# Performance work log

Measured on AMD Instinct MI355X. Metric: run time of the kernel, lower is better.

## Reference

```python
import jax, jax.numpy as jnp
import numpy as np

N_NODES = 50000
N_RAND_EDGES = 800000
N_GRAPHS = 64
IN_DIM, HID, HEADS = 1024, 64, 4
NEG_SLOPE = 0.2  # PyG GATConv default


def setup_inputs() -> dict:
    key = jax.random.key(0)
    ks = jax.random.split(key, 16)
    x = jax.random.normal(ks[0], (N_NODES, IN_DIM), dtype=jnp.float32)
    src = jax.random.randint(ks[1], (N_RAND_EDGES,), 0, N_NODES, dtype=jnp.int32)
    dst = jax.random.randint(ks[2], (N_RAND_EDGES,), 0, N_NODES, dtype=jnp.int32)
    loop = jnp.arange(N_NODES, dtype=jnp.int32)
    # PyG GATConv adds self-loops by default; bake them into edge_index.
    edge_index = jnp.stack([jnp.concatenate([src, loop]), jnp.concatenate([dst, loop])])
    batch = jnp.sort(jax.random.randint(ks[3], (N_NODES,), 0, N_GRAPHS, dtype=jnp.int32))
    s = 0.05
    W1 = jax.random.normal(ks[4], (IN_DIM, HEADS * HID), dtype=jnp.float32) * s
    att_src1 = jax.random.normal(ks[5], (HEADS, HID), dtype=jnp.float32) * s
    att_dst1 = jax.random.normal(ks[6], (HEADS, HID), dtype=jnp.float32) * s
    b1 = jnp.zeros((HEADS * HID,), dtype=jnp.float32)
    W2 = jax.random.normal(ks[7], (HEADS * HID, HID), dtype=jnp.float32) * s
    att_src2 = jax.random.normal(ks[8], (1, HID), dtype=jnp.float32) * s
    att_dst2 = jax.random.normal(ks[9], (1, HID), dtype=jnp.float32) * s
    b2 = jnp.zeros((HID,), dtype=jnp.float32)
    fc_w = jax.random.normal(ks[10], (HID, 2), dtype=jnp.float32) * s
    fc_b = jnp.zeros((2,), dtype=jnp.float32)
    return {"x": x, "edge_index": edge_index, "batch": batch,
            "W1": W1, "att_src1": att_src1, "att_dst1": att_dst1, "b1": b1,
            "W2": W2, "att_src2": att_src2, "att_dst2": att_dst2, "b2": b2,
            "fc_w": fc_w, "fc_b": fc_b}


def gat_conv(x, src, dst, W, a_src, a_dst, b):
    """PyG GATConv (eval mode, concat=True). x:[N,Fin] -> [N, H*C]."""
    N = x.shape[0]
    H, C = a_src.shape
    h = (x @ W).reshape(N, H, C)                      # [N,H,C]
    al_s = jnp.einsum('nhc,hc->nh', h, a_src)         # [N,H]
    al_d = jnp.einsum('nhc,hc->nh', h, a_dst)
    e = jax.nn.leaky_relu(al_s[src] + al_d[dst], NEG_SLOPE)   # [E,H]
    # segment-softmax over edges grouped by destination node
    m = jax.ops.segment_max(e, dst, num_segments=N)           # [N,H]
    w = jnp.exp(e - m[dst])
    denom = jax.ops.segment_sum(w, dst, num_segments=N)
    alpha = w / denom[dst]                                    # [E,H]
    msg = h[src] * alpha[:, :, None]                          # [E,H,C]
    out = jax.ops.segment_sum(msg, dst, num_segments=N)       # [N,H,C]
    return out.reshape(N, H * C) + b


def reference(x, edge_index, batch, W1, att_src1, att_dst1, b1,
              W2, att_src2, att_dst2, b2, fc_w, fc_b):
    src, dst = edge_index[0], edge_index[1]
    # dropout is identity in eval mode
    h = jax.nn.elu(gat_conv(x, src, dst, W1, att_src1, att_dst1, b1))
    h = jax.nn.elu(gat_conv(h, src, dst, W2, att_src2, att_dst2, b2))
    # global mean pool over graphs
    sums = jax.ops.segment_sum(h, batch, num_segments=N_GRAPHS)          # [G,HID]
    cnt = jax.ops.segment_sum(jnp.ones((h.shape[0],), h.dtype), batch,
                              num_segments=N_GRAPHS)
    pooled = sums / jnp.maximum(cnt, 1.0)[:, None]
    return pooled @ fc_w + fc_b                                          # [G,2]
```

## Files before the change

kernel.cpp:

```cpp
#include <hip/hip_runtime.h>
#include <hip/hip_bf16.h>

#define NNODES   50000
#define NGRAPHS  64
#define INDIM    1024
#define HIDC     64
#define HEADS1   4
#define F1       (HEADS1*HIDC)
#define NEG_SLOPE 0.2f

#define WS_COUNTS   0
#define WS_ZEROLEN  50000
#define WS_INDPTR   54208
#define WS_CURSOR   104256
#define WS_CSRSRC   154304
#define WS_CSRDST   1004304
#define WS_BSUM     1854304
#define WS_ALS1     1854368
#define WS_ALD1     2054368
#define WS_ALS2     2254368
#define WS_ALD2     2304368
#define WS_BP       2354368
#define WS_BP2      2485440
#define WS_H1B      2493632
#define WS_X2B      8893632
#define WS_H2B      15293632
#define WS_HFIN     16893632

typedef __attribute__((ext_vector_type(8))) short bf16x8;
typedef __attribute__((ext_vector_type(4))) float f32x4;

__device__ __forceinline__ ushort f2bf(float f) {
    union { float f; uint u; } v; v.f = f;
    uint r = v.u + 0x7fff + ((v.u >> 16) & 1);
    return (ushort)(r >> 16);
}
__device__ __forceinline__ float bf2f(ushort u) {
    union { uint u; float f; } v; v.u = (uint)u << 16; return v.f;
}

__global__ void prep_kernel(const float* __restrict__ W1, const float* __restrict__ W2,
                            ushort* __restrict__ Bp1, ushort* __restrict__ Bp2,
                            int* __restrict__ counts) {
    int b = blockIdx.x;
    int tid = threadIdx.x;
    if (b < 1024) {
        int o = b * 256 + tid;
        int j = o & 7;
        int lane = (o >> 3) & 63;
        int kchunk = (o >> 9) & 31;
        int ntile = o >> 14;
        int k = kchunk * 32 + (lane >> 4) * 8 + j;
        int n = ntile * 16 + (lane & 15);
        Bp1[o] = f2bf(W1[k * 256 + n]);
    } else if (b < 1088) {
        int o = (b - 1024) * 256 + tid;
        int j = o & 7;
        int lane = (o >> 3) & 63;
        int kchunk = (o >> 9) & 7;
        int ntile = o >> 12;
        int k = kchunk * 32 + (lane >> 4) * 8 + j;
        int n = ntile * 16 + (lane & 15);
        Bp2[o] = f2bf(W2[k * 64 + n]);
    } else {
        int i = (b - 1088) * 256 + tid;
        if (i < NNODES) counts[i] = 0;
    }
}

__global__ void hist_kernel(const int* __restrict__ dst, int* __restrict__ counts, int E) {
    int i = blockIdx.x * blockDim.x + threadIdx.x;
    if (i < E) atomicAdd(&counts[dst[i]], 1);
}

__global__ __launch_bounds__(1024) void scan1_kernel(const int* __restrict__ counts,
                                                     int* __restrict__ indptr,
                                                     int* __restrict__ bsum, int N) {
    __shared__ int sm[1024];
    int b = blockIdx.x;
    int i = b * 1024 + (int)threadIdx.x;
    int v = (i < N) ? counts[i] : 0;
    sm[threadIdx.x] = v;
    __syncthreads();
    for (int off = 1; off < 1024; off <<= 1) {
        int t = (threadIdx.x >= (unsigned)off) ? sm[threadIdx.x - off] : 0;
        __syncthreads();
        sm[threadIdx.x] += t;
        __syncthreads();
    }
    if (i < N) indptr[i + 1] = sm[threadIdx.x];
    if (threadIdx.x == 1023) bsum[b] = sm[1023];
}

__global__ void scan2_kernel(int* __restrict__ bsum, int nb) {
    int lane = threadIdx.x;
    int v = (lane < nb) ? bsum[lane] : 0;
    int orig = v;
    #pragma unroll
    for (int off = 1; off < 64; off <<= 1) {
        int t = __shfl_up(v, off, 64);
        if (lane >= off) v += t;
    }
    if (lane < nb) bsum[lane] = v - orig;
}

__global__ __launch_bounds__(1024) void scan3_kernel(const int* __restrict__ counts,
                                                     int* __restrict__ indptr,
                                                     int* __restrict__ cursor,
                                                     const int* __restrict__ bsum, int N) {
    int i = blockIdx.x * 1024 + (int)threadIdx.x;
    if (i == 0) indptr[0] = 0;
    if (i < N) {
        int incl = indptr[i + 1] + bsum[blockIdx.x];
        indptr[i + 1] = incl;
        cursor[i] = incl - counts[i];
    }
}

__global__ void fill_kernel(const int* __restrict__ src, const int* __restrict__ dst,
                            int* __restrict__ cursor, int* __restrict__ csr_src, int E) {
    int i = blockIdx.x * blockDim.x + threadIdx.x;
    if (i < E) {
        int d = dst[i];
        int pos = atomicAdd(&cursor[d], 1);
        csr_src[pos] = src[i];
    }
}

__global__ __launch_bounds__(256) void gemm1_mfma(const float* __restrict__ A,
                                                  const ushort* __restrict__ Bp,
                                                  ushort* __restrict__ C,
                                                  const float* __restrict__ asrc,
                                                  const float* __restrict__ adst,
                                                  float* __restrict__ als,
                                                  float* __restrict__ ald,
                                                  int M) {
    __shared__ __align__(16) ushort Atile[2][128 * 32];
    const int K = 1024, N = 256;
    int tid = threadIdx.x;
    int lane = tid & 63;
    int w = tid >> 6;
    int wm = w >> 1, wn = w & 1;
    int m0 = blockIdx.x * 128;

    const float* srow[4];
    int soff[4];
    #pragma unroll
    for (int l = 0; l < 4; ++l) {
        int slot = l * 256 + tid;
        int m = slot >> 3, hc = slot & 7;
        int c = hc >> 1;
        int row = m0 + m; if (row >= M) row = M - 1;
        srow[l] = A + (size_t)row * K + hc * 4;
        soff[l] = (m * 4 + (c ^ ((m >> 1) & 3))) * 8 + (hc & 1) * 4;
    }
    int afrag_off[4];
    #pragma unroll
    for (int mt = 0; mt < 4; ++mt) {
        int r = wm * 64 + mt * 16 + (lane & 15);
        int cq = lane >> 4;
        afrag_off[mt] = (r * 4 + (cq ^ ((r >> 1) & 3))) * 8;
    }
    const ushort* bbase[8];
    #pragma unroll
    for (int nt = 0; nt < 8; ++nt) {
        int ntile = wn * 8 + nt;
        bbase[nt] = Bp + ((size_t)(ntile * 32) * 64 + lane) * 8;
    }

    f32x4 acc[4][8] = {};
    float4 v[4];
    #pragma unroll
    for (int l = 0; l < 4; ++l) v[l] = *(const float4*)(srow[l]);

    for (int kc = 0; kc < 32; ++kc) {
        ushort* At = Atile[kc & 1];
        #pragma unroll
        for (int l = 0; l < 4; ++l) {
            ushort4 b;
            b.x = f2bf(v[l].x); b.y = f2bf(v[l].y);
            b.z = f2bf(v[l].z); b.w = f2bf(v[l].w);
            *(ushort4*)&At[soff[l]] = b;
        }
        __syncthreads();
        if (kc < 31) {
            #pragma unroll
            for (int l = 0; l < 4; ++l)
                v[l] = *(const float4*)(srow[l] + (kc + 1) * 32);
        }
        bf16x8 afr[4];
        #pragma unroll
        for (int mt = 0; mt < 4; ++mt)
            afr[mt] = *(const bf16x8*)&At[afrag_off[mt]];
        #pragma unroll
        for (int nt = 0; nt < 8; ++nt) {
            bf16x8 bfr = *(const bf16x8*)(bbase[nt] + (size_t)kc * 64 * 8);
            #pragma unroll
            for (int mt = 0; mt < 4; ++mt)
                acc[mt][nt] = __builtin_amdgcn_mfma_f32_16x16x32_bf16(afr[mt], bfr, acc[mt][nt], 0, 0, 0);
        }
    }

    float a_s[8], a_d[8];
    #pragma unroll
    for (int nt = 0; nt < 8; ++nt) {
        int col = wn * 128 + nt * 16 + (lane & 15);
        a_s[nt] = asrc[col];
        a_d[nt] = adst[col];
    }
    #pragma unroll
    for (int mt = 0; mt < 4; ++mt) {
        #pragma unroll
        for (int nt = 0; nt < 8; ++nt) {
            int col = wn * 128 + nt * 16 + (lane & 15);
            #pragma unroll
            for (int r = 0; r < 4; ++r) {
                int row = m0 + wm * 64 + mt * 16 + (lane >> 4) * 4 + r;
                if (row < M) C[(size_t)row * N + col] = f2bf(acc[mt][nt][r]);
            }
        }
        #pragma unroll
        for (int hg = 0; hg < 2; ++hg) {
            int head = wn * 2 + hg;
            #pragma unroll
            for (int r = 0; r < 4; ++r) {
                int row = m0 + wm * 64 + mt * 16 + (lane >> 4) * 4 + r;
                float s = 0.f, d = 0.f;
                #pragma unroll
                for (int q = 0; q < 4; ++q) {
                    float c = acc[mt][4 * hg + q][r];
                    s = fmaf(c, a_s[4 * hg + q], s);
                    d = fmaf(c, a_d[4 * hg + q], d);
                }
                #pragma unroll
                for (int off = 1; off < 16; off <<= 1) {
                    s += __shfl_xor(s, off, 64);
                    d += __shfl_xor(d, off, 64);
                }
                if ((lane & 15) == 0 && row < M) {
                    als[row * 4 + head] = s;
                    ald[row * 4 + head] = d;
                }
            }
        }
    }
}

__global__ __launch_bounds__(256) void gemm2_mfma(const ushort* __restrict__ Ab,
                                                  const ushort* __restrict__ Bp,
                                                  ushort* __restrict__ C,
                                                  const float* __restrict__ asrc,
                                                  const float* __restrict__ adst,
                                                  float* __restrict__ als,
                                                  float* __restrict__ ald,
                                                  int M) {
    int tid = threadIdx.x;
    int lane = tid & 63;
    int w = tid >> 6;
    int m0 = blockIdx.x * 128 + w * 32;

    f32x4 acc[2][4] = {};
    #pragma unroll 2
    for (int kc = 0; kc < 8; ++kc) {
        bf16x8 afr[2];
        #pragma unroll
        for (int mt = 0; mt < 2; ++mt) {
            int r = m0 + mt * 16 + (lane & 15);
            if (r >= M) r = M - 1;
            afr[mt] = *(const bf16x8*)&Ab[(size_t)r * 256 + kc * 32 + (lane >> 4) * 8];
        }
        #pragma unroll
        for (int nt = 0; nt < 4; ++nt) {
            bf16x8 bfr = *(const bf16x8*)&Bp[((nt * 8 + kc) * 64 + lane) * 8];
            acc[0][nt] = __builtin_amdgcn_mfma_f32_16x16x32_bf16(afr[0], bfr, acc[0][nt], 0, 0, 0);
            acc[1][nt] = __builtin_amdgcn_mfma_f32_16x16x32_bf16(afr[1], bfr, acc[1][nt], 0, 0, 0);
        }
    }
    float a_s[4], a_d[4];
    #pragma unroll
    for (int nt = 0; nt < 4; ++nt) {
        a_s[nt] = asrc[nt * 16 + (lane & 15)];
        a_d[nt] = adst[nt * 16 + (lane & 15)];
    }
    #pragma unroll
    for (int mt = 0; mt < 2; ++mt) {
        #pragma unroll
        for (int nt = 0; nt < 4; ++nt) {
            int col = nt * 16 + (lane & 15);
            #pragma unroll
            for (int r = 0; r < 4; ++r) {
                int row = m0 + mt * 16 + (lane >> 4) * 4 + r;
                if (row < M) C[(size_t)row * 64 + col] = f2bf(acc[mt][nt][r]);
            }
        }
        #pragma unroll
        for (int r = 0; r < 4; ++r) {
            int row = m0 + mt * 16 + (lane >> 4) * 4 + r;
            float s = 0.f, d = 0.f;
            #pragma unroll
            for (int nt = 0; nt < 4; ++nt) {
                float c = acc[mt][nt][r];
                s = fmaf(c, a_s[nt], s);
                d = fmaf(c, a_d[nt], d);
            }
            #pragma unroll
            for (int off = 1; off < 16; off <<= 1) {
                s += __shfl_xor(s, off, 64);
                d += __shfl_xor(d, off, 64);
            }
            if ((lane & 15) == 0 && row < M) {
                als[row] = s;
                ald[row] = d;
            }
        }
    }
}

__device__ __forceinline__ float wave_reduce_sum(float v) {
    #pragma unroll
    for (int off = 32; off > 0; off >>= 1) v += __shfl_xor(v, off, 64);
    return v;
}

__device__ __forceinline__ float edge_w(float e) {
    e = (e > 0.f) ? e : NEG_SLOPE * e;
    return __expf(e);
}

__global__ __launch_bounds__(256) void agg1_kernel(const ushort* __restrict__ h,
                                                   const float* __restrict__ als,
                                                   const float* __restrict__ ald,
                                                   const int* __restrict__ indptr,
                                                   const int* __restrict__ csr_src,
                                                   const float* __restrict__ bias,
                                                   ushort* __restrict__ out, int N) {
    __shared__ int   s_s[4][64];
    __shared__ float s_w[4][64][4];
    int wv   = threadIdx.x >> 6;
    int lane = threadIdx.x & 63;
    int n = blockIdx.x * 4 + wv;
    if (n >= N) return;
    int hd = lane >> 4;
    int beg = indptr[n], end = indptr[n + 1];
    float4 aldv = *(const float4*)&ald[n * 4];

    float4 acc = make_float4(0.f, 0.f, 0.f, 0.f);
    float den = 0.f;

    for (int base = beg; base < end; base += 64) {
        int cnt = end - base; if (cnt > 64) cnt = 64;
        if (lane < cnt) {
            int s = csr_src[base + lane];
            s_s[wv][lane] = s;
            float4 av = *(const float4*)&als[s * 4];
            s_w[wv][lane][0] = edge_w(av.x + aldv.x);
            s_w[wv][lane][1] = edge_w(av.y + aldv.y);
            s_w[wv][lane][2] = edge_w(av.z + aldv.z);
            s_w[wv][lane][3] = edge_w(av.w + aldv.w);
        }
        #pragma unroll 4
        for (int e = 0; e < cnt; ++e) {
            int s = s_s[wv][e];
            float wt = s_w[wv][e][hd];
            ushort4 a = *(const ushort4*)&h[(size_t)s * 256 + lane * 4];
            acc.x = fmaf(wt, bf2f(a.x), acc.x);
            acc.y = fmaf(wt, bf2f(a.y), acc.y);
            acc.z = fmaf(wt, bf2f(a.z), acc.z);
            acc.w = fmaf(wt, bf2f(a.w), acc.w);
            den += wt;
        }
    }

    float inv = 1.0f / den;
    float4 bv = *(const float4*)&bias[lane * 4];
    float o0 = acc.x * inv + bv.x, o1 = acc.y * inv + bv.y;
    float o2 = acc.z * inv + bv.z, o3 = acc.w * inv + bv.w;
    o0 = (o0 > 0.f) ? o0 : (__expf(o0) - 1.0f);
    o1 = (o1 > 0.f) ? o1 : (__expf(o1) - 1.0f);
    o2 = (o2 > 0.f) ? o2 : (__expf(o2) - 1.0f);
    o3 = (o3 > 0.f) ? o3 : (__expf(o3) - 1.0f);
    ushort4 ob; ob.x = f2bf(o0); ob.y = f2bf(o1); ob.z = f2bf(o2); ob.w = f2bf(o3);
    *(ushort4*)&out[(size_t)n * 256 + lane * 4] = ob;
}

__global__ __launch_bounds__(256) void agg2_kernel(const ushort* __restrict__ h,
                                                   const float* __restrict__ als,
                                                   const float* __restrict__ ald,
                                                   const int* __restrict__ indptr,
                                                   const int* __restrict__ csr_src,
                                                   const float* __restrict__ bias,
                                                   float* __restrict__ out, int N) {
    __shared__ int   s_s[8][32];
    __shared__ float s_w[8][32];
    int tid = threadIdx.x;
    int sl  = tid >> 5;
    int l32 = tid & 31;
    int n = blockIdx.x * 8 + sl;
    if (n >= N) return;
    int beg = indptr[n], end = indptr[n + 1];
    float ald_n = ald[n];

    float2 acc = make_float2(0.f, 0.f);
    float den = 0.f;

    for (int base = beg; base < end; base += 32) {
        int cnt = end - base; if (cnt > 32) cnt = 32;
        if (l32 < cnt) {
            int s = csr_src[base + l32];
            s_s[sl][l32] = s;
            s_w[sl][l32] = edge_w(als[s] + ald_n);
        }
        #pragma unroll 4
        for (int e = 0; e < cnt; ++e) {
            int s = s_s[sl][e];
            float wt = s_w[sl][e];
            ushort2 hv = *(const ushort2*)&h[(size_t)s * 64 + l32 * 2];
            acc.x = fmaf(wt, bf2f(hv.x), acc.x);
            acc.y = fmaf(wt, bf2f(hv.y), acc.y);
            den += wt;
        }
    }

    float inv = 1.0f / den;
    float o0 = acc.x * inv + bias[l32 * 2];
    float o1 = acc.y * inv + bias[l32 * 2 + 1];
    o0 = (o0 > 0.f) ? o0 : (__expf(o0) - 1.0f);
    o1 = (o1 > 0.f) ? o1 : (__expf(o1) - 1.0f);
    *(float2*)&out[(size_t)n * 64 + l32 * 2] = make_float2(o0, o1);
}

__global__ __launch_bounds__(256) void pool_fc_kernel(const float* __restrict__ hfin,
                                                      const int* __restrict__ batch,
                                                      const float* __restrict__ fc_w,
                                                      const float* __restrict__ fc_b,
                                                      float* __restrict__ out, int N) {
    __shared__ float lacc[4][64];
    int g = blockIdx.x;
    int beg, end;
    {
        int lo = 0, hi = N;
        while (lo < hi) { int mid = (lo + hi) >> 1; if (batch[mid] < g) lo = mid + 1; else hi = mid; }
        beg = lo;
        lo = beg; hi = N;
        while (lo < hi) { int mid = (lo + hi) >> 1; if (batch[mid] < g + 1) lo = mid + 1; else hi = mid; }
        end = lo;
    }
    int lane = threadIdx.x & 63;
    int wv = threadIdx.x >> 6;
    float acc = 0.f;
    for (int n = beg + wv; n < end; n += 4)
        acc += hfin[(size_t)n * 64 + lane];
    lacc[wv][lane] = acc;
    __syncthreads();
    if (wv == 0) {
        float s = lacc[0][lane] + lacc[1][lane] + lacc[2][lane] + lacc[3][lane];
        float cnt = fmaxf((float)(end - beg), 1.0f);
        float pooled = s / cnt;
        float p0 = wave_reduce_sum(pooled * fc_w[lane * 2 + 0]);
        float p1 = wave_reduce_sum(pooled * fc_w[lane * 2 + 1]);
        if (lane == 0) {
            out[g * 2 + 0] = p0 + fc_b[0];
            out[g * 2 + 1] = p1 + fc_b[1];
        }
    }
}

extern "C" void kernel_launch(void* const* d_in, const int* in_sizes, int n_in,
                              void* d_out, int out_size, void* d_ws, size_t ws_size,
                              hipStream_t stream) {
    const float* x      = (const float*)d_in[0];
    const int*   ei     = (const int*)d_in[1];
    const int*   batch  = (const int*)d_in[2];
    const float* W1     = (const float*)d_in[3];
    const float* asrc1  = (const float*)d_in[4];
    const float* adst1  = (const float*)d_in[5];
    const float* b1     = (const float*)d_in[6];
    const float* W2     = (const float*)d_in[7];
    const float* asrc2  = (const float*)d_in[8];
    const float* adst2  = (const float*)d_in[9];
    const float* b2     = (const float*)d_in[10];
    const float* fc_w   = (const float*)d_in[11];
    const float* fc_b   = (const float*)d_in[12];
    float* out          = (float*)d_out;

    const int N = in_sizes[2];
    const int E = in_sizes[1] / 2;
    const int* src = ei;
    const int* dst = ei + E;

    float* ws = (float*)d_ws;
    int*    counts  = (int*)(ws + WS_COUNTS);
    int*    indptr  = (int*)(ws + WS_INDPTR);
    int*    cursor  = (int*)(ws + WS_CURSOR);
    int*    csr_src = (int*)(ws + WS_CSRSRC);
    int*    bsum    = (int*)(ws + WS_BSUM);
    float*  al_s1   = ws + WS_ALS1;
    float*  al_d1   = ws + WS_ALD1;
    float*  al_s2   = ws + WS_ALS2;
    float*  al_d2   = ws + WS_ALD2;
    ushort* bp      = (ushort*)(ws + WS_BP);
    ushort* bp2     = (ushort*)(ws + WS_BP2);
    ushort* h1b     = (ushort*)(ws + WS_H1B);
    ushort* x2b     = (ushort*)(ws + WS_X2B);
    ushort* h2b     = (ushort*)(ws + WS_H2B);
    float*  hfin    = ws + WS_HFIN;

    const int nb = (N + 1023) / 1024;

    prep_kernel<<<1284, 256, 0, stream>>>(W1, W2, bp, bp2, counts);
    hist_kernel<<<(E + 255) / 256, 256, 0, stream>>>(dst, counts, E);
    scan1_kernel<<<nb, 1024, 0, stream>>>(counts, indptr, bsum, N);
    scan2_kernel<<<1, 64, 0, stream>>>(bsum, nb);
    scan3_kernel<<<nb, 1024, 0, stream>>>(counts, indptr, cursor, bsum, N);
    fill_kernel<<<(E + 255) / 256, 256, 0, stream>>>(src, dst, cursor, csr_src, E);
    gemm1_mfma<<<(N + 127) / 128, 256, 0, stream>>>(
        x, bp, h1b, asrc1, adst1, al_s1, al_d1, N);
    agg1_kernel<<<(N + 3) / 4, 256, 0, stream>>>(h1b, al_s1, al_d1, indptr, csr_src, b1, x2b, N);
    gemm2_mfma<<<(N + 127) / 128, 256, 0, stream>>>(
        x2b, bp2, h2b, asrc2, adst2, al_s2, al_d2, N);
    agg2_kernel<<<(N + 7) / 8, 256, 0, stream>>>(h2b, al_s2, al_d2, indptr, csr_src, b2, hfin, N);
    pool_fc_kernel<<<NGRAPHS, 256, 0, stream>>>(hfin, batch, fc_w, fc_b, out, N);
}
```

Baseline: 575.9 us.

## Pre-convert x to bf16 in separate pass and drop LDS staging in gemm1

Adds a standalone kernel converting the fp32 node features to bf16 in workspace, then gemm1 reads bf16 A fragments directly from global memory instead of converting and staging through double-buffered shared memory with barriers. This removes in-loop conversion and syncthreads from the GEMM. It adds an extra full pass over the large input (read fp32, write bf16, read bf16 again) and relies on cache for the uncoalesced per-lane row fragment loads.

```diff
diff --git a/kernel.cpp b/kernel.cpp
--- a/kernel.cpp
+++ b/kernel.cpp
@@ -26,6 +26,7 @@
 #define WS_X2B      8893632
 #define WS_H2B      15293632
 #define WS_HFIN     16893632
+#define WS_XB       20093632
 
 typedef __attribute__((ext_vector_type(8))) short bf16x8;
 typedef __attribute__((ext_vector_type(4))) float f32x4;
@@ -37,6 +38,20 @@
 }
 __device__ __forceinline__ float bf2f(ushort u) {
     union { uint u; float f; } v; v.u = (uint)u << 16; return v.f;
+}
+
+__global__ void cvt_x_kernel(const float* __restrict__ x, ushort* __restrict__ xb,
+                             long n8) {
+    long i = blockIdx.x * (long)blockDim.x + threadIdx.x;
+    long stride = (long)gridDim.x * blockDim.x;
+    for (; i < n8; i += stride) {
+        const float4* p = (const float4*)(x + i * 8);
+        float4 a = p[0], b = p[1];
+        union { ushort u[8]; uint4 v; } o;
+        o.u[0] = f2bf(a.x); o.u[1] = f2bf(a.y); o.u[2] = f2bf(a.z); o.u[3] = f2bf(a.w);
+        o.u[4] = f2bf(b.x); o.u[5] = f2bf(b.y); o.u[6] = f2bf(b.z); o.u[7] = f2bf(b.w);
+        *(uint4*)(xb + i * 8) = o.v;
+    }
 }
 
 __global__ void prep_kernel(const float* __restrict__ W1, const float* __restrict__ W2,
@@ -127,7 +142,7 @@
     }
 }
 
-__global__ __launch_bounds__(256) void gemm1_mfma(const float* __restrict__ A,
+__global__ __launch_bounds__(256) void gemm1_mfma(const ushort* __restrict__ Ab,
                                                   const ushort* __restrict__ Bp,
                                                   ushort* __restrict__ C,
                                                   const float* __restrict__ asrc,
@@ -135,7 +150,6 @@
                                                   float* __restrict__ als,
                                                   float* __restrict__ ald,
                                                   int M) {
-    __shared__ __align__(16) ushort Atile[2][128 * 32];
     const int K = 1024, N = 256;
     int tid = threadIdx.x;
     int lane = tid & 63;
@@ -143,23 +157,12 @@
     int wm = w >> 1, wn = w & 1;
     int m0 = blockIdx.x * 128;
 
-    const float* srow[4];
-    int soff[4];
-    #pragma unroll
-    for (int l = 0; l < 4; ++l) {
-        int slot = l * 256 + tid;
-        int m = slot >> 3, hc = slot & 7;
-        int c = hc >> 1;
-        int row = m0 + m; if (row >= M) row = M - 1;
-        srow[l] = A + (size_t)row * K + hc * 4;
-        soff[l] = (m * 4 + (c ^ ((m >> 1) & 3))) * 8 + (hc & 1) * 4;
-    }
-    int afrag_off[4];
+    const ushort* arow[4];
     #pragma unroll
     for (int mt = 0; mt < 4; ++mt) {
-        int r = wm * 64 + mt * 16 + (lane & 15);
-        int cq = lane >> 4;
-        afrag_off[mt] = (r * 4 + (cq ^ ((r >> 1) & 3))) * 8;
+        int r = m0 + wm * 64 + mt * 16 + (lane & 15);
+        if (r >= M) r = M - 1;
+        arow[mt] = Ab + (size_t)r * K + (lane >> 4) * 8;
     }
     const ushort* bbase[8];
     #pragma unroll
@@ -169,32 +172,16 @@
     }
 
     f32x4 acc[4][8] = {};
-    float4 v[4];
-    #pragma unroll
-    for (int l = 0; l < 4; ++l) v[l] = *(const float4*)(srow[l]);
-
+
+    #pragma unroll 2
     for (int kc = 0; kc < 32; ++kc) {
-        ushort* At = Atile[kc & 1];
-        #pragma unroll
-        for (int l = 0; l < 4; ++l) {
-            ushort4 b;
-            b.x = f2bf(v[l].x); b.y = f2bf(v[l].y);
-            b.z = f2bf(v[l].z); b.w = f2bf(v[l].w);
-            *(ushort4*)&At[soff[l]] = b;
-        }
-        __syncthreads();
-        if (kc < 31) {
-            #pragma unroll
-            for (int l = 0; l < 4; ++l)
-                v[l] = *(const float4*)(srow[l] + (kc + 1) * 32);
-        }
         bf16x8 afr[4];
         #pragma unroll
         for (int mt = 0; mt < 4; ++mt)
-            afr[mt] = *(const bf16x8*)&At[afrag_off[mt]];
+            afr[mt] = *(const bf16x8*)(arow[mt] + kc * 32);
         #pragma unroll
         for (int nt = 0; nt < 8; ++nt) {
-            bf16x8 bfr = *(const bf16x8*)(bbase[nt] + (size_t)kc * 64 * 8);
+            bf16x8 bfr = *(const bf16x8*)(bbase[nt] + (size_t)kc * 512);
             #pragma unroll
             for (int mt = 0; mt < 4; ++mt)
                 acc[mt][nt] = __builtin_amdgcn_mfma_f32_16x16x32_bf16(afr[mt], bfr, acc[mt][nt], 0, 0, 0);
@@ -504,17 +491,19 @@
     ushort* x2b     = (ushort*)(ws + WS_X2B);
     ushort* h2b     = (ushort*)(ws + WS_H2B);
     float*  hfin    = ws + WS_HFIN;
+    ushort* xb      = (ushort*)(ws + WS_XB);
 
     const int nb = (N + 1023) / 1024;
 
     prep_kernel<<<1284, 256, 0, stream>>>(W1, W2, bp, bp2, counts);
+    cvt_x_kernel<<<2048, 256, 0, stream>>>(x, xb, (long)N * (INDIM / 8));
     hist_kernel<<<(E + 255) / 256, 256, 0, stream>>>(dst, counts, E);
     scan1_kernel<<<nb, 1024, 0, stream>>>(counts, indptr, bsum, N);
     scan2_kernel<<<1, 64, 0, stream>>>(bsum, nb);
     scan3_kernel<<<nb, 1024, 0, stream>>>(counts, indptr, cursor, bsum, N);
     fill_kernel<<<(E + 255) / 256, 256, 0, stream>>>(src, dst, cursor, csr_src, E);
     gemm1_mfma<<<(N + 127) / 128, 256, 0, stream>>>(
-        x, bp, h1b, asrc1, adst1, al_s1, al_d1, N);
+        xb, bp, h1b, asrc1, adst1, al_s1, al_d1, N);
     agg1_kernel<<<(N + 3) / 4, 256, 0, stream>>>(h1b, al_s1, al_d1, indptr, csr_src, b1, x2b, N);
     gemm2_mfma<<<(N + 127) / 128, 256, 0, stream>>>(
         x2b, bp2, h2b, asrc2, adst2, al_s2, al_d2, N);
```

Measured after the change: 694.6 us. 1.21x slower.
